# Performance work log

Hardware: AMD Instinct MI355X
Metric: run time of the kernel (lower is better)

Reference implementation:

```python
import jax, jax.numpy as jnp
import numpy as np

B, N, D = 256, 196, 768  # batch, num_patches (14x14 grid), patch_dim (16*16*3)


def setup_inputs() -> dict:
    key = jax.random.key(0)
    k1, k2 = jax.random.split(key)
    features = jax.random.normal(k1, (B, N, D), dtype=jnp.float32)
    position_logits = jax.random.normal(k2, (B, N, N), dtype=jnp.float32)
    return {"features": features, "position_logits": position_logits}


def _rearrange_patches(patches, pos):
    # Deterministic gather form: for each target slot p, take the LARGEST j with
    # pos[i, j] == p, else leave the zero-init.
    b, n, d = patches.shape
    j_ids = jnp.arange(n, dtype=jnp.int32)
    match = pos[:, :, None] == jnp.arange(n)[None, None, :]          # [B, j, p]
    winner = jnp.max(jnp.where(match, j_ids[None, :, None], -1), axis=1)  # [B, p]
    gathered = jnp.take_along_axis(patches, jnp.clip(winner, 0)[:, :, None], axis=1)
    return jnp.where(winner[:, :, None] >= 0, gathered, jnp.zeros((), patches.dtype))


def reference(features, position_logits):
    b, n, d = features.shape
    g = int(n ** 0.5)
    # _get_position_predictions: argmax / max-softmax over dim=1 (position classes)
    pos = jnp.argmax(position_logits, axis=1)                         # [B, N] int
    confidence = jnp.max(jax.nn.softmax(position_logits, axis=1), axis=1)  # [B, N]
    # _rearrange_patches (scatter by predicted position)
    patches = _rearrange_patches(features, pos)
    # _smooth_edges: 3-tap average over interior patch indices, reading originals
    mid = (patches[:, :-2] + patches[:, 1:-1] + patches[:, 2:]) / 3.0
    patches = jnp.concatenate([patches[:, :1], mid, patches[:, -1:]], axis=1)
    # _reconstruct_image: [B, g, g, D] -> [B, D, g, g]
    img = patches.reshape(b, g, g, d).transpose(0, 3, 1, 2)
    return img, confidence
```

## Files before the change

### kernel.cpp

```cpp
#include <hip/hip_runtime.h>
#include <math.h>

#define BB 256
#define NN 196
#define DD 768
#define TDK 32
#define NTILES (DD / TDK)
#define PSTRIDE 204
#define NW 16

typedef float f32x4 __attribute__((ext_vector_type(4)));

__global__ __launch_bounds__(1024) void fused_kernel(
    const float* __restrict__ features,
    const float* __restrict__ logits,
    float* __restrict__ img,
    float* __restrict__ conf_out)
{
    const int b = blockIdx.x;
    const int t = threadIdx.x;

    __shared__ float sm[NW][NN];
    __shared__ float ss[NW][NN];
    __shared__ int   si[NW][NN];
    __shared__ int   winner_s[NN];
    __shared__ float tile[TDK][PSTRIDE];

    const int wv = t >> 6;
    const int l  = t & 63;

    if (t < NN) winner_s[t] = -1;

    {
        const int i0 = (49 * wv) >> 2;
        const int i1 = (49 * (wv + 1)) >> 2;
        if (l < 49) {
            const float* basep = logits + (size_t)b * NN * NN + 4 * l;
            f32x4 m = {-INFINITY, -INFINITY, -INFINITY, -INFINITY};
            f32x4 s = {0.f, 0.f, 0.f, 0.f};
            int4 idx = make_int4(0, 0, 0, 0);
            #pragma unroll 4
            for (int i = i0; i < i1; ++i) {
                const f32x4 x = *reinterpret_cast<const f32x4*>(basep + (size_t)i * NN);
                f32x4 mn;
                mn.x = fmaxf(m.x, x.x); mn.y = fmaxf(m.y, x.y);
                mn.z = fmaxf(m.z, x.z); mn.w = fmaxf(m.w, x.w);
                idx.x = (x.x > m.x) ? i : idx.x;
                idx.y = (x.y > m.y) ? i : idx.y;
                idx.z = (x.z > m.z) ? i : idx.z;
                idx.w = (x.w > m.w) ? i : idx.w;
                s.x = s.x * __expf(m.x - mn.x) + __expf(x.x - mn.x);
                s.y = s.y * __expf(m.y - mn.y) + __expf(x.y - mn.y);
                s.z = s.z * __expf(m.z - mn.z) + __expf(x.z - mn.z);
                s.w = s.w * __expf(m.w - mn.w) + __expf(x.w - mn.w);
                m = mn;
            }
            const int c = 4 * l;
            sm[wv][c + 0] = m.x; ss[wv][c + 0] = s.x; si[wv][c + 0] = idx.x;
            sm[wv][c + 1] = m.y; ss[wv][c + 1] = s.y; si[wv][c + 1] = idx.y;
            sm[wv][c + 2] = m.z; ss[wv][c + 2] = s.z; si[wv][c + 2] = idx.z;
            sm[wv][c + 3] = m.w; ss[wv][c + 3] = s.w; si[wv][c + 3] = idx.w;
        }
    }
    __syncthreads();

    if (t < NN) {
        const int j = t;
        float m = -INFINITY;
        int idx = 0;
        #pragma unroll
        for (int ww = 0; ww < NW; ++ww) {
            const float mg = sm[ww][j];
            if (mg > m) { m = mg; idx = si[ww][j]; }
        }
        float s = 0.0f;
        #pragma unroll
        for (int ww = 0; ww < NW; ++ww)
            s += ss[ww][j] * __expf(sm[ww][j] - m);
        conf_out[b * NN + j] = 1.0f / s;
        atomicMax(&winner_s[idx], j);
    }
    __syncthreads();

    const float* fb = features + (size_t)b * NN * DD;
    float* ob = img + (size_t)b * DD * NN;

    const int q1_ok = (t < 1568 - 1024);
    const int r0 = t >> 3;
    const int d40 = (t & 7) * 4;
    const int r1 = (t + 1024) >> 3;
    const int d41 = ((t + 1024) & 7) * 4;

    const int w0 = winner_s[r0];
    const int w1 = q1_ok ? winner_s[r1] : -1;

    const f32x4 zero = {0.f, 0.f, 0.f, 0.f};
    f32x4 v0 = zero, v1 = zero, nv0 = zero, nv1 = zero;

    if (w0 >= 0) v0 = *reinterpret_cast<const f32x4*>(fb + (size_t)w0 * DD + d40);
    if (w1 >= 0) v1 = *reinterpret_cast<const f32x4*>(fb + (size_t)w1 * DD + d41);

    for (int k = 0; k < NTILES; ++k) {
        tile[d40 + 0][r0] = v0.x;
        tile[d40 + 1][r0] = v0.y;
        tile[d40 + 2][r0] = v0.z;
        tile[d40 + 3][r0] = v0.w;
        if (q1_ok) {
            tile[d41 + 0][r1] = v1.x;
            tile[d41 + 1][r1] = v1.y;
            tile[d41 + 2][r1] = v1.z;
            tile[d41 + 3][r1] = v1.w;
        }

        if (k + 1 < NTILES) {
            const int d0n = (k + 1) * TDK;
            nv0 = zero; nv1 = zero;
            if (w0 >= 0) nv0 = *reinterpret_cast<const f32x4*>(fb + (size_t)w0 * DD + d0n + d40);
            if (w1 >= 0) nv1 = *reinterpret_cast<const f32x4*>(fb + (size_t)w1 * DD + d0n + d41);
        }
        __syncthreads();

        const int d0 = k * TDK;
        #pragma unroll
        for (int it = 0; it < 2; ++it) {
            const int q = t + 1024 * it;
            if (q < TDK * 49) {
                const int d = q / 49;
                const int c = q - 49 * d;
                const int p0 = 4 * c;
                const f32x4 ctr = *reinterpret_cast<const f32x4*>(&tile[d][p0]);
                const float left  = tile[d][p0 > 0 ? p0 - 1 : 0];
                const float right = tile[d][p0 + 4 < NN ? p0 + 4 : NN - 1];
                f32x4 o;
                o.x = (p0 == 0)          ? ctr.x : (left  + ctr.x + ctr.y) * (1.0f / 3.0f);
                o.y = (ctr.x + ctr.y + ctr.z) * (1.0f / 3.0f);
                o.z = (ctr.y + ctr.z + ctr.w) * (1.0f / 3.0f);
                o.w = (p0 + 3 == NN - 1) ? ctr.w : (ctr.z + ctr.w + right) * (1.0f / 3.0f);
                float* dst = ob + (size_t)(d0 + d) * NN + p0;
                __builtin_nontemporal_store(o, reinterpret_cast<f32x4*>(dst));
            }
        }
        v0 = nv0; v1 = nv1;
        __syncthreads();
    }
}

extern "C" void kernel_launch(void* const* d_in, const int* in_sizes, int n_in,
                              void* d_out, int out_size, void* d_ws, size_t ws_size,
                              hipStream_t stream) {
    const float* features = (const float*)d_in[0];
    const float* logits   = (const float*)d_in[1];

    float* out  = (float*)d_out;
    float* img  = out;
    float* conf = out + (size_t)BB * DD * NN;

    fused_kernel<<<BB, 1024, 0, stream>>>(features, logits, img, conf);
}
```

Baseline: 50.53 us.

## Split D dimension across two blocks per batch and swizzle shared tile

The launch now uses a 2D grid with two blocks per batch, each handling half of the feature dimension with 512 threads instead of one 1024-thread block. Each block recomputes the argmax and softmax over the logits redundantly, using 8 waves instead of 16, and only the first half-block writes the confidence output. The shared transpose tile moves to an XOR-swizzled layout so that the transposed writes avoid bank conflicts. The goal is more resident blocks and better latency hiding, at the cost of reading the logits twice.

```diff
diff --git a/kernel.cpp b/kernel.cpp
--- a/kernel.cpp
+++ b/kernel.cpp
@@ -5,26 +5,30 @@
 #define NN 196
 #define DD 768
 #define TDK 32
-#define NTILES (DD / TDK)
-#define PSTRIDE 204
-#define NW 16
+#define NHALF 2
+#define DHALF (DD / NHALF)
+#define NTILES (DHALF / TDK)
+#define SROW 224
+#define NW 8
+#define NITEMS (NN * 8)
 
 typedef float f32x4 __attribute__((ext_vector_type(4)));
 
-__global__ __launch_bounds__(1024) void fused_kernel(
+__global__ __launch_bounds__(512) void fused_kernel(
     const float* __restrict__ features,
     const float* __restrict__ logits,
     float* __restrict__ img,
     float* __restrict__ conf_out)
 {
     const int b = blockIdx.x;
+    const int h = blockIdx.y;
     const int t = threadIdx.x;
 
     __shared__ float sm[NW][NN];
     __shared__ float ss[NW][NN];
     __shared__ int   si[NW][NN];
     __shared__ int   winner_s[NN];
-    __shared__ float tile[TDK][PSTRIDE];
+    __shared__ float tile[TDK * SROW];
 
     const int wv = t >> 6;
     const int l  = t & 63;
@@ -32,8 +36,8 @@
     if (t < NN) winner_s[t] = -1;
 
     {
-        const int i0 = (49 * wv) >> 2;
-        const int i1 = (49 * (wv + 1)) >> 2;
+        const int i0 = (49 * wv) >> 1;
+        const int i1 = (49 * (wv + 1)) >> 1;
         if (l < 49) {
             const float* basep = logits + (size_t)b * NN * NN + 4 * l;
             f32x4 m = {-INFINITY, -INFINITY, -INFINITY, -INFINITY};
@@ -77,70 +81,82 @@
         #pragma unroll
         for (int ww = 0; ww < NW; ++ww)
             s += ss[ww][j] * __expf(sm[ww][j] - m);
-        conf_out[b * NN + j] = 1.0f / s;
+        if (h == 0) conf_out[b * NN + j] = 1.0f / s;
         atomicMax(&winner_s[idx], j);
     }
     __syncthreads();
 
     const float* fb = features + (size_t)b * NN * DD;
-    float* ob = img + (size_t)b * DD * NN;
+    const int D0 = h * DHALF;
+    float* ob = img + (size_t)b * DD * NN + (size_t)D0 * NN;
 
-    const int q1_ok = (t < 1568 - 1024);
-    const int r0 = t >> 3;
-    const int d40 = (t & 7) * 4;
-    const int r1 = (t + 1024) >> 3;
-    const int d41 = ((t + 1024) & 7) * 4;
-
-    const int w0 = winner_s[r0];
-    const int w1 = q1_ok ? winner_s[r1] : -1;
+    int  rr[4], k4[4], wn[4];
+    bool act[4];
+    #pragma unroll
+    for (int i = 0; i < 4; ++i) {
+        const int item = t + 512 * i;
+        act[i] = (item < NITEMS);
+        rr[i]  = act[i] ? (item >> 3) : 0;
+        k4[i]  = (item & 7) * 4;
+        wn[i]  = act[i] ? winner_s[rr[i]] : -1;
+    }
 
     const f32x4 zero = {0.f, 0.f, 0.f, 0.f};
-    f32x4 v0 = zero, v1 = zero, nv0 = zero, nv1 = zero;
+    f32x4 cur[4], nxt[4];
+    #pragma unroll
+    for (int i = 0; i < 4; ++i)
+        cur[i] = (wn[i] >= 0)
+            ? *reinterpret_cast<const f32x4*>(fb + (size_t)wn[i] * DD + D0 + k4[i])
+            : zero;
 
-    if (w0 >= 0) v0 = *reinterpret_cast<const f32x4*>(fb + (size_t)w0 * DD + d40);
-    if (w1 >= 0) v1 = *reinterpret_cast<const f32x4*>(fb + (size_t)w1 * DD + d41);
-
-    for (int k = 0; k < NTILES; ++k) {
-        tile[d40 + 0][r0] = v0.x;
-        tile[d40 + 1][r0] = v0.y;
-        tile[d40 + 2][r0] = v0.z;
-        tile[d40 + 3][r0] = v0.w;
-        if (q1_ok) {
-            tile[d41 + 0][r1] = v1.x;
-            tile[d41 + 1][r1] = v1.y;
-            tile[d41 + 2][r1] = v1.z;
-            tile[d41 + 3][r1] = v1.w;
+    for (int kt = 0; kt < NTILES; ++kt) {
+        #pragma unroll
+        for (int i = 0; i < 4; ++i) {
+            if (act[i]) {
+                const int r  = rr[i];
+                const int kb = k4[i] >> 2;
+                const int col = (((r >> 2) ^ kb) << 2) + (r & 3);
+                tile[(k4[i] + 0) * SROW + col] = cur[i].x;
+                tile[(k4[i] + 1) * SROW + col] = cur[i].y;
+                tile[(k4[i] + 2) * SROW + col] = cur[i].z;
+                tile[(k4[i] + 3) * SROW + col] = cur[i].w;
+            }
         }
-
-        if (k + 1 < NTILES) {
-            const int d0n = (k + 1) * TDK;
-            nv0 = zero; nv1 = zero;
-            if (w0 >= 0) nv0 = *reinterpret_cast<const f32x4*>(fb + (size_t)w0 * DD + d0n + d40);
-            if (w1 >= 0) nv1 = *reinterpret_cast<const f32x4*>(fb + (size_t)w1 * DD + d0n + d41);
+        #pragma unroll
+        for (int i = 0; i < 4; ++i) nxt[i] = zero;
+        if (kt + 1 < NTILES) {
+            const int dn = D0 + (kt + 1) * TDK;
+            #pragma unroll
+            for (int i = 0; i < 4; ++i)
+                if (wn[i] >= 0)
+                    nxt[i] = *reinterpret_cast<const f32x4*>(fb + (size_t)wn[i] * DD + dn + k4[i]);
         }
         __syncthreads();
 
-        const int d0 = k * TDK;
+        const int dg0 = kt * TDK;
         #pragma unroll
-        for (int it = 0; it < 2; ++it) {
-            const int q = t + 1024 * it;
+        for (int it = 0; it < 4; ++it) {
+            const int q = t + 512 * it;
             if (q < TDK * 49) {
-                const int d = q / 49;
-                const int c = q - 49 * d;
+                const int dl  = q / 49;
+                const int c   = q - 49 * dl;
+                const int key = (dl >> 2) & 7;
+                const float* row = &tile[dl * SROW];
+                const f32x4 ctr = *reinterpret_cast<const f32x4*>(row + ((c ^ key) << 2));
+                const float left  = (c > 0)  ? row[(((c - 1) ^ key) << 2) + 3] : 0.0f;
+                const float right = (c < 48) ? row[ ((c + 1) ^ key) << 2      ] : 0.0f;
                 const int p0 = 4 * c;
-                const f32x4 ctr = *reinterpret_cast<const f32x4*>(&tile[d][p0]);
-                const float left  = tile[d][p0 > 0 ? p0 - 1 : 0];
-                const float right = tile[d][p0 + 4 < NN ? p0 + 4 : NN - 1];
                 f32x4 o;
                 o.x = (p0 == 0)          ? ctr.x : (left  + ctr.x + ctr.y) * (1.0f / 3.0f);
                 o.y = (ctr.x + ctr.y + ctr.z) * (1.0f / 3.0f);
                 o.z = (ctr.y + ctr.z + ctr.w) * (1.0f / 3.0f);
                 o.w = (p0 + 3 == NN - 1) ? ctr.w : (ctr.z + ctr.w + right) * (1.0f / 3.0f);
-                float* dst = ob + (size_t)(d0 + d) * NN + p0;
+                float* dst = ob + (size_t)(dg0 + dl) * NN + p0;
                 __builtin_nontemporal_store(o, reinterpret_cast<f32x4*>(dst));
             }
         }
-        v0 = nv0; v1 = nv1;
+        #pragma unroll
+        for (int i = 0; i < 4; ++i) cur[i] = nxt[i];
         __syncthreads();
     }
 }
@@ -155,5 +171,6 @@
     float* img  = out;
     float* conf = out + (size_t)BB * DD * NN;
 
-    fused_kernel<<<BB, 1024, 0, stream>>>(features, logits, img, conf);
+    dim3 grid(BB, NHALF);
+    fused_kernel<<<grid, 512, 0, stream>>>(features, logits, img, conf);
 }
```

After: 50.92 us. No clear change (+0.8%).

## Double-buffer transpose tile with XOR swizzle and drop second barrier

Applied to the files above, without the earlier changes.

The single LDS transpose tile becomes two buffers that alternate per iteration, which removes the trailing __syncthreads in each of the 24 tile iterations. The buffers share storage through a union with the softmax-reduction scratch so LDS use does not grow. The tile layout is XOR-swizzled on 4-float column groups to cut bank conflicts on the transposed writes while keeping the vector reads aligned. The costs are extra index arithmetic and a reliance on a single barrier per iteration for correctness across the two buffers.

```diff
diff --git a/kernel.cpp b/kernel.cpp
--- a/kernel.cpp
+++ b/kernel.cpp
@@ -6,7 +6,8 @@
 #define DD 768
 #define TDK 32
 #define NTILES (DD / TDK)
-#define PSTRIDE 204
+#define SROW 224
+#define NITEMS (NN * 8)
 #define NW 16
 
 typedef float f32x4 __attribute__((ext_vector_type(4)));
@@ -20,11 +21,11 @@
     const int b = blockIdx.x;
     const int t = threadIdx.x;
 
-    __shared__ float sm[NW][NN];
-    __shared__ float ss[NW][NN];
-    __shared__ int   si[NW][NN];
-    __shared__ int   winner_s[NN];
-    __shared__ float tile[TDK][PSTRIDE];
+    __shared__ union {
+        struct { float sm[NW][NN]; float ss[NW][NN]; int si[NW][NN]; } a;
+        float tiles[2][TDK * SROW];
+    } u;
+    __shared__ int winner_s[NN];
 
     const int wv = t >> 6;
     const int l  = t & 63;
@@ -56,10 +57,10 @@
                 m = mn;
             }
             const int c = 4 * l;
-            sm[wv][c + 0] = m.x; ss[wv][c + 0] = s.x; si[wv][c + 0] = idx.x;
-            sm[wv][c + 1] = m.y; ss[wv][c + 1] = s.y; si[wv][c + 1] = idx.y;
-            sm[wv][c + 2] = m.z; ss[wv][c + 2] = s.z; si[wv][c + 2] = idx.z;
-            sm[wv][c + 3] = m.w; ss[wv][c + 3] = s.w; si[wv][c + 3] = idx.w;
+            u.a.sm[wv][c + 0] = m.x; u.a.ss[wv][c + 0] = s.x; u.a.si[wv][c + 0] = idx.x;
+            u.a.sm[wv][c + 1] = m.y; u.a.ss[wv][c + 1] = s.y; u.a.si[wv][c + 1] = idx.y;
+            u.a.sm[wv][c + 2] = m.z; u.a.ss[wv][c + 2] = s.z; u.a.si[wv][c + 2] = idx.z;
+            u.a.sm[wv][c + 3] = m.w; u.a.ss[wv][c + 3] = s.w; u.a.si[wv][c + 3] = idx.w;
         }
     }
     __syncthreads();
@@ -70,13 +71,13 @@
         int idx = 0;
         #pragma unroll
         for (int ww = 0; ww < NW; ++ww) {
-            const float mg = sm[ww][j];
-            if (mg > m) { m = mg; idx = si[ww][j]; }
+            const float mg = u.a.sm[ww][j];
+            if (mg > m) { m = mg; idx = u.a.si[ww][j]; }
         }
         float s = 0.0f;
         #pragma unroll
         for (int ww = 0; ww < NW; ++ww)
-            s += ss[ww][j] * __expf(sm[ww][j] - m);
+            s += u.a.ss[ww][j] * __expf(u.a.sm[ww][j] - m);
         conf_out[b * NN + j] = 1.0f / s;
         atomicMax(&winner_s[idx], j);
     }
@@ -85,63 +86,68 @@
     const float* fb = features + (size_t)b * NN * DD;
     float* ob = img + (size_t)b * DD * NN;
 
-    const int q1_ok = (t < 1568 - 1024);
-    const int r0 = t >> 3;
-    const int d40 = (t & 7) * 4;
-    const int r1 = (t + 1024) >> 3;
-    const int d41 = ((t + 1024) & 7) * 4;
+    const int  r0  = t >> 3;
+    const int  k40 = (t & 7) * 4;
+    const bool a1  = (t + 1024) < NITEMS;
+    const int  r1  = (t + 1024) >> 3;
+    const int  k41 = ((t + 1024) & 7) * 4;
 
     const int w0 = winner_s[r0];
-    const int w1 = q1_ok ? winner_s[r1] : -1;
+    const int w1 = a1 ? winner_s[r1] : -1;
+
+    const int col0 = (((r0 >> 2) ^ (k40 >> 2)) << 2) + (r0 & 3);
+    const int col1 = (((r1 >> 2) ^ (k41 >> 2)) << 2) + (r1 & 3);
 
     const f32x4 zero = {0.f, 0.f, 0.f, 0.f};
-    f32x4 v0 = zero, v1 = zero, nv0 = zero, nv1 = zero;
+    f32x4 cur0, cur1, nxt0, nxt1;
+    cur0 = (w0 >= 0) ? *reinterpret_cast<const f32x4*>(fb + (size_t)w0 * DD + k40) : zero;
+    cur1 = (w1 >= 0) ? *reinterpret_cast<const f32x4*>(fb + (size_t)w1 * DD + k41) : zero;
 
-    if (w0 >= 0) v0 = *reinterpret_cast<const f32x4*>(fb + (size_t)w0 * DD + d40);
-    if (w1 >= 0) v1 = *reinterpret_cast<const f32x4*>(fb + (size_t)w1 * DD + d41);
+    for (int kt = 0; kt < NTILES; ++kt) {
+        float* buf = u.tiles[kt & 1];
 
-    for (int k = 0; k < NTILES; ++k) {
-        tile[d40 + 0][r0] = v0.x;
-        tile[d40 + 1][r0] = v0.y;
-        tile[d40 + 2][r0] = v0.z;
-        tile[d40 + 3][r0] = v0.w;
-        if (q1_ok) {
-            tile[d41 + 0][r1] = v1.x;
-            tile[d41 + 1][r1] = v1.y;
-            tile[d41 + 2][r1] = v1.z;
-            tile[d41 + 3][r1] = v1.w;
+        buf[(k40 + 0) * SROW + col0] = cur0.x;
+        buf[(k40 + 1) * SROW + col0] = cur0.y;
+        buf[(k40 + 2) * SROW + col0] = cur0.z;
+        buf[(k40 + 3) * SROW + col0] = cur0.w;
+        if (a1) {
+            buf[(k41 + 0) * SROW + col1] = cur1.x;
+            buf[(k41 + 1) * SROW + col1] = cur1.y;
+            buf[(k41 + 2) * SROW + col1] = cur1.z;
+            buf[(k41 + 3) * SROW + col1] = cur1.w;
         }
 
-        if (k + 1 < NTILES) {
-            const int d0n = (k + 1) * TDK;
-            nv0 = zero; nv1 = zero;
-            if (w0 >= 0) nv0 = *reinterpret_cast<const f32x4*>(fb + (size_t)w0 * DD + d0n + d40);
-            if (w1 >= 0) nv1 = *reinterpret_cast<const f32x4*>(fb + (size_t)w1 * DD + d0n + d41);
+        nxt0 = zero; nxt1 = zero;
+        if (kt + 1 < NTILES) {
+            const int dn = (kt + 1) * TDK;
+            if (w0 >= 0) nxt0 = *reinterpret_cast<const f32x4*>(fb + (size_t)w0 * DD + dn + k40);
+            if (w1 >= 0) nxt1 = *reinterpret_cast<const f32x4*>(fb + (size_t)w1 * DD + dn + k41);
         }
+
         __syncthreads();
 
-        const int d0 = k * TDK;
+        const int dg0 = kt * TDK;
         #pragma unroll
         for (int it = 0; it < 2; ++it) {
             const int q = t + 1024 * it;
-            if (q < TDK * 49) {
-                const int d = q / 49;
-                const int c = q - 49 * d;
+            if (q < NITEMS) {
+                const int dl  = q / 49;
+                const int c   = q - 49 * dl;
+                const int key = (dl >> 2) & 7;
+                const float* row = &buf[dl * SROW];
+                const f32x4 ctr = *reinterpret_cast<const f32x4*>(row + ((c ^ key) << 2));
+                const float left  = (c > 0)  ? row[(((c - 1) ^ key) << 2) + 3] : 0.0f;
+                const float right = (c < 48) ? row[ ((c + 1) ^ key) << 2      ] : 0.0f;
                 const int p0 = 4 * c;
-                const f32x4 ctr = *reinterpret_cast<const f32x4*>(&tile[d][p0]);
-                const float left  = tile[d][p0 > 0 ? p0 - 1 : 0];
-                const float right = tile[d][p0 + 4 < NN ? p0 + 4 : NN - 1];
                 f32x4 o;
                 o.x = (p0 == 0)          ? ctr.x : (left  + ctr.x + ctr.y) * (1.0f / 3.0f);
                 o.y = (ctr.x + ctr.y + ctr.z) * (1.0f / 3.0f);
                 o.z = (ctr.y + ctr.z + ctr.w) * (1.0f / 3.0f);
                 o.w = (p0 + 3 == NN - 1) ? ctr.w : (ctr.z + ctr.w + right) * (1.0f / 3.0f);
-                float* dst = ob + (size_t)(d0 + d) * NN + p0;
-                __builtin_nontemporal_store(o, reinterpret_cast<f32x4*>(dst));
+                __builtin_nontemporal_store(o, reinterpret_cast<f32x4*>(ob + (size_t)(dg0 + dl) * NN + p0));
             }
         }
-        v0 = nv0; v1 = nv1;
-        __syncthreads();
+        cur0 = nxt0; cur1 = nxt1;
     }
 }
 
```

New measurement: 50.49 us. About the same (-0.1%).
